# Kernel tuning notes

Hardware: AMD Instinct MI355X
Metric: run time of the kernel (lower is better)

The kernel has to match this reference:

```python
import jax, jax.numpy as jnp
import numpy as np

N_HEADS = 16
HEAD_DIM = 64
D_MODEL = N_HEADS * HEAD_DIM
MASK_NUM = -2.0**32 + 1.0
LN_EPS = 1e-8


def setup_inputs() -> dict:
    key = jax.random.key(0)
    ks = jax.random.split(key, 6)
    B, S = 2, 2048
    queries = jax.random.normal(ks[0], (B, S, D_MODEL), dtype=jnp.float32)
    keys = jax.random.normal(ks[1], (B, S, D_MODEL), dtype=jnp.float32)
    values = jax.random.normal(ks[2], (B, S, D_MODEL), dtype=jnp.float32)
    lim = np.sqrt(6.0 / (D_MODEL + D_MODEL)).astype(np.float32)  # glorot_uniform
    Wq = jax.random.uniform(ks[3], (D_MODEL, D_MODEL), jnp.float32, -lim, lim)
    Wk = jax.random.uniform(ks[4], (D_MODEL, D_MODEL), jnp.float32, -lim, lim)
    Wv = jax.random.uniform(ks[5], (D_MODEL, D_MODEL), jnp.float32, -lim, lim)
    gamma = jnp.ones((D_MODEL,), jnp.float32)
    beta = jnp.zeros((D_MODEL,), jnp.float32)
    return {"queries": queries, "keys": keys, "values": values,
            "Wq": Wq, "Wk": Wk, "Wv": Wv, "gamma": gamma, "beta": beta}


def _split_heads(x):
    # [B, S, H*dh] -> tf.split(axis=2)+concat(axis=0) order: [H*B, S, dh]
    B, S, _ = x.shape
    return x.reshape(B, S, N_HEADS, HEAD_DIM).transpose(2, 0, 1, 3).reshape(N_HEADS * B, S, HEAD_DIM)


def _merge_heads(x, B):
    # [H*B, S, dh] -> [B, S, H*dh]
    S = x.shape[1]
    return x.reshape(N_HEADS, B, S, HEAD_DIM).transpose(1, 2, 0, 3).reshape(B, S, D_MODEL)


def reference(queries, keys, values, Wq, Wk, Wv, gamma, beta):
    B = queries.shape[0]
    q = _split_heads(queries @ Wq)   # [HB, Sq, dh]
    k = _split_heads(keys @ Wk)      # [HB, Sk, dh]
    v = _split_heads(values @ Wv)    # [HB, Sk, dh]

    scores = jnp.einsum('bqd,bkd->bqk', q, k) / jnp.float32(np.sqrt(HEAD_DIM))
    # key padding mask: positions whose projected key is all-zero
    kmask = jnp.sign(jnp.sum(jnp.abs(k), axis=-1))  # [HB, Sk]
    scores = jnp.where(kmask[:, None, :] == 0, jnp.float32(MASK_NUM), scores)
    attn = jax.nn.softmax(scores, axis=-1)
    # query mask: zero out rows whose projected query is all-zero
    qmask = jnp.sign(jnp.sum(jnp.abs(q), axis=-1))  # [HB, Sq]
    attn = attn * qmask[:, :, None]
    att_out = jnp.einsum('bqk,bkd->bqd', attn, v)   # [HB, Sq, dh]
    att_out = _merge_heads(att_out, B)               # [B, Sq, D]

    x = att_out + queries
    mean = jnp.mean(x, axis=-1, keepdims=True)
    var = jnp.mean((x - mean) ** 2, axis=-1, keepdims=True)
    norm = (x - mean) / jnp.sqrt(var + LN_EPS)
    return gamma * norm + beta
```

## Files before the change

kernel.cpp:

```cpp
#include <hip/hip_runtime.h>

#define DM   1024
#define SEQ  2048
#define NH   16
#define HD   64
#define ROWS 4096

typedef unsigned short u16;
typedef unsigned int   u32;
typedef __attribute__((ext_vector_type(8))) __bf16 bf16x8;
typedef __attribute__((ext_vector_type(4))) float  f32x4;
typedef __attribute__((ext_vector_type(16))) float f32x16;

__device__ __forceinline__ u16 f2bf(float f) {
  u32 u = __builtin_bit_cast(u32, f);
  u += 0x7fffu + ((u >> 16) & 1u);
  return (u16)(u >> 16);
}

__device__ __forceinline__ void async16(const void* g, void* lds) {
  __builtin_amdgcn_global_load_lds((const __attribute__((address_space(1))) u32*)g,
                                   (__attribute__((address_space(3))) u32*)lds, 16, 0, 0);
}


__global__ __launch_bounds__(256) void k_cvt_act(const float* __restrict__ q,
                                                 const float* __restrict__ k,
                                                 const float* __restrict__ v,
                                                 u16* __restrict__ dst) {
  const float* src = blockIdx.z == 0 ? q : (blockIdx.z == 1 ? k : v);
  u16* d = dst + (size_t)blockIdx.z * ((size_t)ROWS * DM);
  size_t i = ((size_t)blockIdx.x * 256 + threadIdx.x) * 8;
  float4 a = *(const float4*)(src + i);
  float4 b = *(const float4*)(src + i + 4);
  u32 w0 = (u32)f2bf(a.x) | ((u32)f2bf(a.y) << 16);
  u32 w1 = (u32)f2bf(a.z) | ((u32)f2bf(a.w) << 16);
  u32 w2 = (u32)f2bf(b.x) | ((u32)f2bf(b.y) << 16);
  u32 w3 = (u32)f2bf(b.z) | ((u32)f2bf(b.w) << 16);
  uint4 o4; o4.x = w0; o4.y = w1; o4.z = w2; o4.w = w3;
  *(uint4*)(d + i) = o4;
}

__global__ __launch_bounds__(256) void k_cvt_wt(const float* __restrict__ Wq,
                                                const float* __restrict__ Wk,
                                                const float* __restrict__ Wv,
                                                u16* __restrict__ wt) {
  __shared__ float t[32][33];
  const float* W = blockIdx.z == 0 ? Wq : (blockIdx.z == 1 ? Wk : Wv);
  u16* D = wt + (size_t)blockIdx.z * (DM * DM);
  int bx = blockIdx.x * 32, by = blockIdx.y * 32;
  int x = threadIdx.x, y = threadIdx.y;
  for (int i = 0; i < 32; i += 8) t[y + i][x] = W[(size_t)(by + y + i) * DM + bx + x];
  __syncthreads();
  for (int i = 0; i < 32; i += 8) D[(size_t)(bx + y + i) * DM + by + x] = f2bf(t[x][y + i]);
}


__global__ __launch_bounds__(256) void k_gemm(const u16* __restrict__ Abase,
                                              const u16* __restrict__ Btbase,
                                              u16* __restrict__ Cbase) {
  __shared__ u16 As[128 * 32];
  __shared__ u16 Bs[128 * 32];
  const int z = blockIdx.z;
  const u16* A  = Abase  + (size_t)z * ((size_t)ROWS * DM);
  const u16* Bt = Btbase + (size_t)z * (DM * DM);
  u16* C        = Cbase  + (size_t)z * ((size_t)ROWS * DM);
  const float sc = (z == 0) ? 0.18033688011112043f : 1.0f;
  int tid = threadIdx.x, w = tid >> 6, l = tid & 63;
  int fr = l & 15, fq = l >> 4;
  int bid = blockIdx.y * 8 + blockIdx.x;
  int nb  = (bid & 7) * 32 + (bid >> 3);
  int m0 = (nb >> 3) * 128, n0 = (nb & 7) * 128;
  int wr = (w >> 1) * 64, wc = (w & 1) * 64;
  f32x4 acc[4][4];
  for (int i = 0; i < 4; ++i) for (int j = 0; j < 4; ++j) acc[i][j] = (f32x4){0.f, 0.f, 0.f, 0.f};

  for (int k0 = 0; k0 < DM; k0 += 32) {
    __syncthreads();
    for (int c = 0; c < 2; ++c) {
      int loff = (c * 4 + w) * 1024;
      int eoff = (loff >> 1) + l * 8;
      int row = eoff >> 5;
      int blk = (eoff & 31) >> 3;
      int gblk = blk ^ ((row >> 1) & 3);
      async16(A  + (size_t)(m0 + row) * DM + k0 + (gblk << 3), (char*)As + loff);
      async16(Bt + (size_t)(n0 + row) * DM + k0 + (gblk << 3), (char*)Bs + loff);
    }
    __syncthreads();
    bf16x8 af[4], bf[4];
    for (int i = 0; i < 4; ++i) {
      int row = wr + i * 16 + fr;
      af[i] = *(const bf16x8*)(As + row * 32 + ((fq ^ ((row >> 1) & 3)) << 3));
    }
    for (int j = 0; j < 4; ++j) {
      int row = wc + j * 16 + fr;
      bf[j] = *(const bf16x8*)(Bs + row * 32 + ((fq ^ ((row >> 1) & 3)) << 3));
    }
    for (int i = 0; i < 4; ++i)
      for (int j = 0; j < 4; ++j)
        acc[i][j] = __builtin_amdgcn_mfma_f32_16x16x32_bf16(af[i], bf[j], acc[i][j], 0, 0, 0);
  }
  for (int i = 0; i < 4; ++i)
    for (int j = 0; j < 4; ++j)
      for (int jj = 0; jj < 4; ++jj) {
        int row = m0 + wr + i * 16 + fq * 4 + jj;
        int col = n0 + wc + j * 16 + fr;
        C[(size_t)row * DM + col] = f2bf(acc[i][j][jj] * sc);
      }
}


__global__ __launch_bounds__(256) void k_vt(const u16* __restrict__ vproj,
                                            u16* __restrict__ vt) {
  __shared__ u16 t[64][64];
  int y = blockIdx.y;
  int h = y >> 1, b = y & 1;
  int s0 = blockIdx.x * 64;
  int tid = threadIdx.x;
  for (int c = 0; c < 2; ++c) {
    int rr = c * 32 + (tid >> 3);
    int blk = tid & 7;
    uint4 vv = *(const uint4*)(vproj + (size_t)(b * SEQ + s0 + rr) * DM + h * 64 + blk * 8);
    *(uint4*)(&t[rr][((blk ^ (rr & 7)) * 8)]) = vv;
  }
  __syncthreads();
  for (int c = 0; c < 2; ++c) {
    int d = c * 32 + (tid >> 3);
    int p = tid & 7;
    int B = p ^ (d & 7);
    int g = B >> 1, half = B & 1;
    u16 tmp[8];
    for (int j = 0; j < 8; ++j) {
      int kj = (j < 4) ? (4 * half + j) : (8 + 4 * half + (j - 4));
      int ss = 16 * g + kj;
      tmp[j] = t[ss][((d >> 3) ^ (ss & 7)) * 8 + (d & 7)];
    }
    *(uint4*)(vt + (size_t)(y * 64 + d) * SEQ + s0 + p * 8) = *(uint4*)tmp;
  }
}


__global__ __launch_bounds__(256, 2) void k_attn(const u16* __restrict__ Qp,
                                                 const u16* __restrict__ Kp,
                                                 const u16* __restrict__ Vt,
                                                 u16* __restrict__ attb) {
  __shared__ u16 lds[20480];
  const int tid = threadIdx.x, w = tid >> 6, l = tid & 63;
  const int lrow = l & 31, h = l >> 5;
  const int kh = w & 1, qg = w >> 1;
  const int g = blockIdx.x;
  const int vy = (g & 7) * 4 + ((g >> 3) & 3);
  const int vx = g >> 5;
  const int head = vy >> 1, b = vy & 1;
  const int hcol = head * 64;
  const int q0w = vx * 128 + qg * 64;

  bf16x8 qb00, qb01, qb02, qb03, qb10, qb11, qb12, qb13;
  {
    const u16* qr0 = Qp + (size_t)(b * SEQ + q0w + lrow) * DM + hcol + h * 8;
    qb00 = *(const bf16x8*)(qr0);
    qb01 = *(const bf16x8*)(qr0 + 16);
    qb02 = *(const bf16x8*)(qr0 + 32);
    qb03 = *(const bf16x8*)(qr0 + 48);
    const u16* qr1 = Qp + (size_t)(b * SEQ + q0w + 32 + lrow) * DM + hcol + h * 8;
    qb10 = *(const bf16x8*)(qr1);
    qb11 = *(const bf16x8*)(qr1 + 16);
    qb12 = *(const bf16x8*)(qr1 + 32);
    qb13 = *(const bf16x8*)(qr1 + 48);
  }

  const int sw = lrow & 7;
  const int kbase = kh * 4096 + lrow * 128;
  const int B0 = kbase + (((0 + h) ^ sw) << 4);
  const int B1 = kbase + (((2 + h) ^ sw) << 4);
  const int B2 = kbase + (((4 + h) ^ sw) << 4);
  const int B3 = kbase + (((6 + h) ^ sw) << 4);

  const int vfb = lrow * 128;
  const int V0 = vfb + (((4 * kh + 0 + h) ^ sw) << 4);
  const int V1 = vfb + (((4 * kh + 2 + h) ^ sw) << 4);

  const int ldo0 = w * 1024, ldo1 = (4 + w) * 1024;
  const int e0 = (ldo0 >> 1) + l * 8, e1 = (ldo1 >> 1) + l * 8;
  const int r0 = e0 >> 6, r1 = e1 >> 6;
  const int kb0 = ((e0 & 63) >> 3) ^ (r0 & 7), kb1 = ((e1 & 63) >> 3) ^ (r1 & 7);
  const u32 koff0 = (u32)((b * SEQ + r0) * DM + hcol + kb0 * 8);
  const u32 koff1 = (u32)((b * SEQ + r1) * DM + hcol + kb1 * 8);
  const u32 voff0 = (u32)((vy * 64 + r0) * SEQ + (e0 & 63));
  const u32 voff1 = (u32)((vy * 64 + r1) * SEQ + (e1 & 63));

  const f32x16 kzero = {};
  f32x16 ot00 = {}, ot01 = {}, ot10 = {}, ot11 = {};
  float lacc0 = 0.f, lacc1 = 0.f;
  bf16x8 pb00 = {}, pb01 = {}, pb10 = {}, pb11 = {};

  char* base = (char*)lds;
  async16(Kp + koff0, base + ldo0);
  async16(Kp + koff1, base + ldo1);
  async16(Vt + voff0, base + 16384 + ldo0);
  async16(Vt + voff1, base + 16384 + ldo1);

  int vwr = 1, vcr = 0, vrd = 2;
  for (int t = 0; t < SEQ / 64; ++t) {
    {
      u32 u = (t + 1 < SEQ / 64) ? (u32)(t + 1) : (u32)(SEQ / 64 - 1);
      u32 kadv = u * (64 * DM);
      u32 vadv = u * 64;
      char* kd = base + ((t + 1) & 1) * 8192;
      char* vd = base + 16384 + vwr * 8192;
      async16(Kp + kadv + koff0, kd + ldo0);
      async16(Kp + kadv + koff1, kd + ldo1);
      async16(Vt + vadv + voff0, vd + ldo0);
      async16(Vt + vadv + voff1, vd + ldo1);
    }
    asm volatile("s_waitcnt vmcnt(6)" ::: "memory");
    __builtin_amdgcn_s_barrier();
    asm volatile("" ::: "memory");

    const char* Kb = base + (t & 1) * 8192;
    bf16x8 a0 = *(const bf16x8*)(Kb + B0);
    bf16x8 a1 = *(const bf16x8*)(Kb + B1);
    bf16x8 a2 = *(const bf16x8*)(Kb + B2);
    bf16x8 a3 = *(const bf16x8*)(Kb + B3);
    __builtin_amdgcn_s_setprio(1);
    f32x16 st0 = __builtin_amdgcn_mfma_f32_32x32x16_bf16(a0, qb00, kzero, 0, 0, 0);
    f32x16 st1 = __builtin_amdgcn_mfma_f32_32x32x16_bf16(a0, qb10, kzero, 0, 0, 0);
    st0 = __builtin_amdgcn_mfma_f32_32x32x16_bf16(a1, qb01, st0, 0, 0, 0);
    st1 = __builtin_amdgcn_mfma_f32_32x32x16_bf16(a1, qb11, st1, 0, 0, 0);
    st0 = __builtin_amdgcn_mfma_f32_32x32x16_bf16(a2, qb02, st0, 0, 0, 0);
    st1 = __builtin_amdgcn_mfma_f32_32x32x16_bf16(a2, qb12, st1, 0, 0, 0);
    st0 = __builtin_amdgcn_mfma_f32_32x32x16_bf16(a3, qb03, st0, 0, 0, 0);
    st1 = __builtin_amdgcn_mfma_f32_32x32x16_bf16(a3, qb13, st1, 0, 0, 0);
    __builtin_amdgcn_s_setprio(0);

    if (t) {
      const char* Vb = base + 16384 + vrd * 8192;
      bf16x8 vf0 = *(const bf16x8*)(Vb + V0);
      bf16x8 vf1 = *(const bf16x8*)(Vb + V1);
      bf16x8 vf2 = *(const bf16x8*)(Vb + 4096 + V0);
      bf16x8 vf3 = *(const bf16x8*)(Vb + 4096 + V1);
      __builtin_amdgcn_s_setprio(1);
      ot00 = __builtin_amdgcn_mfma_f32_32x32x16_bf16(vf0, pb00, ot00, 0, 0, 0);
      ot10 = __builtin_amdgcn_mfma_f32_32x32x16_bf16(vf0, pb10, ot10, 0, 0, 0);
      ot00 = __builtin_amdgcn_mfma_f32_32x32x16_bf16(vf1, pb01, ot00, 0, 0, 0);
      ot10 = __builtin_amdgcn_mfma_f32_32x32x16_bf16(vf1, pb11, ot10, 0, 0, 0);
      ot01 = __builtin_amdgcn_mfma_f32_32x32x16_bf16(vf2, pb00, ot01, 0, 0, 0);
      ot11 = __builtin_amdgcn_mfma_f32_32x32x16_bf16(vf2, pb10, ot11, 0, 0, 0);
      ot01 = __builtin_amdgcn_mfma_f32_32x32x16_bf16(vf3, pb01, ot01, 0, 0, 0);
      ot11 = __builtin_amdgcn_mfma_f32_32x32x16_bf16(vf3, pb11, ot11, 0, 0, 0);
      __builtin_amdgcn_s_setprio(0);
    }

    {
      f32x16 p;
#pragma unroll
      for (int i = 0; i < 16; ++i) p[i] = __builtin_amdgcn_exp2f(st0[i]);
      float s0 = (p[0] + p[1]) + (p[2] + p[3]);
      float s1 = (p[4] + p[5]) + (p[6] + p[7]);
      float s2 = (p[8] + p[9]) + (p[10] + p[11]);
      float s3 = (p[12] + p[13]) + (p[14] + p[15]);
      lacc0 += (s0 + s1) + (s2 + s3);
#pragma unroll
      for (int j = 0; j < 8; ++j) { pb00[j] = (__bf16)p[j]; pb01[j] = (__bf16)p[8 + j]; }
    }
    {
      f32x16 p;
#pragma unroll
      for (int i = 0; i < 16; ++i) p[i] = __builtin_amdgcn_exp2f(st1[i]);
      float s0 = (p[0] + p[1]) + (p[2] + p[3]);
      float s1 = (p[4] + p[5]) + (p[6] + p[7]);
      float s2 = (p[8] + p[9]) + (p[10] + p[11]);
      float s3 = (p[12] + p[13]) + (p[14] + p[15]);
      lacc1 += (s0 + s1) + (s2 + s3);
#pragma unroll
      for (int j = 0; j < 8; ++j) { pb10[j] = (__bf16)p[j]; pb11[j] = (__bf16)p[8 + j]; }
    }

    asm volatile("" ::: "memory");
    __builtin_amdgcn_s_barrier();
    asm volatile("" ::: "memory");

    int tmp = vrd; vrd = vcr; vcr = vwr; vwr = tmp;
  }

  asm volatile("s_waitcnt vmcnt(0)" ::: "memory");
  __builtin_amdgcn_s_barrier();
  asm volatile("" ::: "memory");
  {
    const char* Vb = base + 16384 + vrd * 8192;
    bf16x8 vf0 = *(const bf16x8*)(Vb + V0);
    bf16x8 vf1 = *(const bf16x8*)(Vb + V1);
    bf16x8 vf2 = *(const bf16x8*)(Vb + 4096 + V0);
    bf16x8 vf3 = *(const bf16x8*)(Vb + 4096 + V1);
    ot00 = __builtin_amdgcn_mfma_f32_32x32x16_bf16(vf0, pb00, ot00, 0, 0, 0);
    ot10 = __builtin_amdgcn_mfma_f32_32x32x16_bf16(vf0, pb10, ot10, 0, 0, 0);
    ot00 = __builtin_amdgcn_mfma_f32_32x32x16_bf16(vf1, pb01, ot00, 0, 0, 0);
    ot10 = __builtin_amdgcn_mfma_f32_32x32x16_bf16(vf1, pb11, ot10, 0, 0, 0);
    ot01 = __builtin_amdgcn_mfma_f32_32x32x16_bf16(vf2, pb00, ot01, 0, 0, 0);
    ot11 = __builtin_amdgcn_mfma_f32_32x32x16_bf16(vf2, pb10, ot11, 0, 0, 0);
    ot01 = __builtin_amdgcn_mfma_f32_32x32x16_bf16(vf3, pb01, ot01, 0, 0, 0);
    ot11 = __builtin_amdgcn_mfma_f32_32x32x16_bf16(vf3, pb11, ot11, 0, 0, 0);
  }
  lacc0 += __shfl_xor(lacc0, 32);
  lacc1 += __shfl_xor(lacc1, 32);

  __syncthreads();
  float* mrg = (float*)lds;
  const int slot = qg * 4352;
  if (kh) {
#pragma unroll
    for (int r = 0; r < 16; ++r) {
      mrg[slot + r * 64 + l] = ot00[r];
      mrg[slot + (16 + r) * 64 + l] = ot01[r];
      mrg[slot + (32 + r) * 64 + l] = ot10[r];
      mrg[slot + (48 + r) * 64 + l] = ot11[r];
    }
    mrg[slot + 4096 + l] = lacc0;
    mrg[slot + 4160 + l] = lacc1;
  }
  __syncthreads();
  if (!kh) {
    float inv0 = 1.f / (lacc0 + mrg[slot + 4096 + l]);
    float inv1 = 1.f / (lacc1 + mrg[slot + 4160 + l]);
    u16* orow0 = attb + (size_t)(b * SEQ + q0w + lrow) * DM + hcol + 4 * h;
    u16* orow1 = attb + (size_t)(b * SEQ + q0w + 32 + lrow) * DM + hcol + 4 * h;
#pragma unroll
    for (int G = 0; G < 4; ++G) {
      uint2 o;
      o.x = (u32)f2bf((ot00[4*G+0] + mrg[slot + (4*G+0)*64 + l]) * inv0)
          | ((u32)f2bf((ot00[4*G+1] + mrg[slot + (4*G+1)*64 + l]) * inv0) << 16);
      o.y = (u32)f2bf((ot00[4*G+2] + mrg[slot + (4*G+2)*64 + l]) * inv0)
          | ((u32)f2bf((ot00[4*G+3] + mrg[slot + (4*G+3)*64 + l]) * inv0) << 16);
      *(uint2*)(orow0 + 8 * G) = o;
      uint2 o1;
      o1.x = (u32)f2bf((ot01[4*G+0] + mrg[slot + (16+4*G+0)*64 + l]) * inv0)
           | ((u32)f2bf((ot01[4*G+1] + mrg[slot + (16+4*G+1)*64 + l]) * inv0) << 16);
      o1.y = (u32)f2bf((ot01[4*G+2] + mrg[slot + (16+4*G+2)*64 + l]) * inv0)
           | ((u32)f2bf((ot01[4*G+3] + mrg[slot + (16+4*G+3)*64 + l]) * inv0) << 16);
      *(uint2*)(orow0 + 32 + 8 * G) = o1;
      uint2 o2;
      o2.x = (u32)f2bf((ot10[4*G+0] + mrg[slot + (32+4*G+0)*64 + l]) * inv1)
           | ((u32)f2bf((ot10[4*G+1] + mrg[slot + (32+4*G+1)*64 + l]) * inv1) << 16);
      o2.y = (u32)f2bf((ot10[4*G+2] + mrg[slot + (32+4*G+2)*64 + l]) * inv1)
           | ((u32)f2bf((ot10[4*G+3] + mrg[slot + (32+4*G+3)*64 + l]) * inv1) << 16);
      *(uint2*)(orow1 + 8 * G) = o2;
      uint2 o3;
      o3.x = (u32)f2bf((ot11[4*G+0] + mrg[slot + (48+4*G+0)*64 + l]) * inv1)
           | ((u32)f2bf((ot11[4*G+1] + mrg[slot + (48+4*G+1)*64 + l]) * inv1) << 16);
      o3.y = (u32)f2bf((ot11[4*G+2] + mrg[slot + (48+4*G+2)*64 + l]) * inv1)
           | ((u32)f2bf((ot11[4*G+3] + mrg[slot + (48+4*G+3)*64 + l]) * inv1) << 16);
      *(uint2*)(orow1 + 32 + 8 * G) = o3;
    }
  }
}


__global__ __launch_bounds__(256) void k_ln(const u16* __restrict__ attb,
                                            const float* __restrict__ qin,
                                            const float* __restrict__ gamma,
                                            const float* __restrict__ beta,
                                            float* __restrict__ out) {
  __shared__ float rsum[4], rsum2[4];
  int row = blockIdx.x, t = threadIdx.x;
  size_t off = (size_t)row * DM + t * 4;
  uint2 av = *(const uint2*)(attb + off);
  float4 a;
  a.x = __builtin_bit_cast(float, av.x << 16);
  a.y = __builtin_bit_cast(float, av.x & 0xffff0000u);
  a.z = __builtin_bit_cast(float, av.y << 16);
  a.w = __builtin_bit_cast(float, av.y & 0xffff0000u);
  float4 q = *(const float4*)(qin + off);
  float4 x; x.x = a.x + q.x; x.y = a.y + q.y; x.z = a.z + q.z; x.w = a.w + q.w;
  float s = x.x + x.y + x.z + x.w;
  float s2 = x.x * x.x + x.y * x.y + x.z * x.z + x.w * x.w;
  for (int o2 = 1; o2 < 64; o2 <<= 1) { s += __shfl_xor(s, o2); s2 += __shfl_xor(s2, o2); }
  int w = t >> 6, l = t & 63;
  if (l == 0) { rsum[w] = s; rsum2[w] = s2; }
  __syncthreads();
  s = rsum[0] + rsum[1] + rsum[2] + rsum[3];
  s2 = rsum2[0] + rsum2[1] + rsum2[2] + rsum2[3];
  float mean = s * (1.f / DM);
  float var = s2 * (1.f / DM) - mean * mean;
  float rstd = rsqrtf(var + 1e-8f);
  float4 g = *(const float4*)(gamma + t * 4);
  float4 be = *(const float4*)(beta + t * 4);
  float4 r;
  r.x = (x.x - mean) * rstd * g.x + be.x;
  r.y = (x.y - mean) * rstd * g.y + be.y;
  r.z = (x.z - mean) * rstd * g.z + be.z;
  r.w = (x.w - mean) * rstd * g.w + be.w;
  *(float4*)(out + off) = r;
}


extern "C" void kernel_launch(void* const* d_in, const int* in_sizes, int n_in,
                              void* d_out, int out_size, void* d_ws, size_t ws_size,
                              hipStream_t stream) {
  (void)in_sizes; (void)n_in; (void)out_size; (void)ws_size;
  const float* q     = (const float*)d_in[0];
  const float* k     = (const float*)d_in[1];
  const float* v     = (const float*)d_in[2];
  const float* Wq    = (const float*)d_in[3];
  const float* Wk    = (const float*)d_in[4];
  const float* Wv    = (const float*)d_in[5];
  const float* gamma = (const float*)d_in[6];
  const float* beta  = (const float*)d_in[7];
  float* out = (float*)d_out;
  char* ws = (char*)d_ws;

  const size_t ACT_B = 3ull * ROWS * DM * 2;
  const size_t WT_B  = 3ull * DM * DM * 2;

  u16* actb  = (u16*)ws;
  u16* wtb   = (u16*)(ws + ACT_B);
  u16* projb = (u16*)(ws + ACT_B + WT_B);
  u16* vt    = (u16*)ws;
  u16* attb  = (u16*)(ws + 8ull * 1024 * 1024);

  k_cvt_act<<<dim3(2048, 1, 3), 256, 0, stream>>>(q, k, v, actb);
  k_cvt_wt<<<dim3(32, 32, 3), dim3(32, 8), 0, stream>>>(Wq, Wk, Wv, wtb);
  k_gemm<<<dim3(8, 32, 3), 256, 0, stream>>>(actb, wtb, projb);
  k_vt<<<dim3(SEQ / 64, NH * 2), 256, 0, stream>>>(projb + 2ull * ROWS * DM, vt);
  k_attn<<<512, 256, 0, stream>>>(projb, projb + (size_t)ROWS * DM, vt, attb);
  k_ln<<<ROWS, 256, 0, stream>>>(attb, q, gamma, beta, out);
}
```

Measured before the change: 108.7 us.

## Enlarge projection GEMM tiles to 256x256 with double-buffered async LDS loads

The QKV projection GEMM now uses 512-thread blocks computing 256x256 output tiles with a K-step of 64, in place of 128x128 tiles with K-step 32. LDS is double-buffered so the next tile's global-to-LDS async loads are in flight during the MFMAs on the current tile, with partial vmcnt waits and raw barriers. s_setprio is raised around the MFMA bursts. The goal is better operand reuse and overlap of memory with compute. The cost is 128 KB of LDS per block and only 192 blocks over 256 CUs, so part of the GPU sits idle.

New measurement: 110.5 us. Within noise of the previous version (+1.7%).

```diff
diff --git a/kernel.cpp b/kernel.cpp
--- a/kernel.cpp
+++ b/kernel.cpp
@@ -56,51 +56,83 @@
 }
 
 
-__global__ __launch_bounds__(256) void k_gemm(const u16* __restrict__ Abase,
+__global__ __launch_bounds__(512) void k_gemm(const u16* __restrict__ Abase,
                                               const u16* __restrict__ Btbase,
                                               u16* __restrict__ Cbase) {
-  __shared__ u16 As[128 * 32];
-  __shared__ u16 Bs[128 * 32];
+  __shared__ u16 As[2][256 * 64];
+  __shared__ u16 Bs[2][256 * 64];
   const int z = blockIdx.z;
   const u16* A  = Abase  + (size_t)z * ((size_t)ROWS * DM);
   const u16* Bt = Btbase + (size_t)z * (DM * DM);
   u16* C        = Cbase  + (size_t)z * ((size_t)ROWS * DM);
   const float sc = (z == 0) ? 0.18033688011112043f : 1.0f;
-  int tid = threadIdx.x, w = tid >> 6, l = tid & 63;
-  int fr = l & 15, fq = l >> 4;
-  int bid = blockIdx.y * 8 + blockIdx.x;
-  int nb  = (bid & 7) * 32 + (bid >> 3);
-  int m0 = (nb >> 3) * 128, n0 = (nb & 7) * 128;
-  int wr = (w >> 1) * 64, wc = (w & 1) * 64;
-  f32x4 acc[4][4];
-  for (int i = 0; i < 4; ++i) for (int j = 0; j < 4; ++j) acc[i][j] = (f32x4){0.f, 0.f, 0.f, 0.f};
-
-  for (int k0 = 0; k0 < DM; k0 += 32) {
-    __syncthreads();
-    for (int c = 0; c < 2; ++c) {
-      int loff = (c * 4 + w) * 1024;
-      int eoff = (loff >> 1) + l * 8;
-      int row = eoff >> 5;
-      int blk = (eoff & 31) >> 3;
-      int gblk = blk ^ ((row >> 1) & 3);
-      async16(A  + (size_t)(m0 + row) * DM + k0 + (gblk << 3), (char*)As + loff);
-      async16(Bt + (size_t)(n0 + row) * DM + k0 + (gblk << 3), (char*)Bs + loff);
-    }
-    __syncthreads();
-    bf16x8 af[4], bf[4];
-    for (int i = 0; i < 4; ++i) {
-      int row = wr + i * 16 + fr;
-      af[i] = *(const bf16x8*)(As + row * 32 + ((fq ^ ((row >> 1) & 3)) << 3));
-    }
-    for (int j = 0; j < 4; ++j) {
-      int row = wc + j * 16 + fr;
-      bf[j] = *(const bf16x8*)(Bs + row * 32 + ((fq ^ ((row >> 1) & 3)) << 3));
-    }
-    for (int i = 0; i < 4; ++i)
-      for (int j = 0; j < 4; ++j)
-        acc[i][j] = __builtin_amdgcn_mfma_f32_16x16x32_bf16(af[i], bf[j], acc[i][j], 0, 0, 0);
-  }
-  for (int i = 0; i < 4; ++i)
+  const int tid = threadIdx.x, w = tid >> 6, l = tid & 63;
+  const int fr = l & 15, fq = l >> 4;
+  int bid = blockIdx.y * 4 + blockIdx.x;
+  int nb  = (bid & 7) * 8 + (bid >> 3);
+  int m0 = (nb >> 2) * 256, n0 = (nb & 3) * 256;
+  int wr = (w >> 2) * 128, wc = (w & 3) * 64;
+  f32x4 acc[8][4];
+  for (int i = 0; i < 8; ++i) for (int j = 0; j < 4; ++j) acc[i][j] = (f32x4){0.f, 0.f, 0.f, 0.f};
+
+  u32 aoff[4], boff[4];
+#pragma unroll
+  for (int i = 0; i < 4; ++i) {
+    int c = i * 512 + tid;
+    int row = c >> 3, blk = c & 7;
+    int gblk = blk ^ (row & 7);
+    aoff[i] = (u32)((m0 + row) * DM + gblk * 8);
+    boff[i] = (u32)((n0 + row) * DM + gblk * 8);
+  }
+
+#pragma unroll
+  for (int i = 0; i < 4; ++i) {
+    async16(A  + aoff[i], (char*)As[0] + (i * 512 + tid) * 16);
+    async16(Bt + boff[i], (char*)Bs[0] + (i * 512 + tid) * 16);
+  }
+
+  for (int t = 0; t < 16; ++t) {
+    const int cur = t & 1, nxt = cur ^ 1;
+    {
+      u32 kk = (t + 1 < 16) ? (u32)(t + 1) * 64u : 15u * 64u;
+#pragma unroll
+      for (int i = 0; i < 4; ++i) {
+        async16(A  + kk + aoff[i], (char*)As[nxt] + (i * 512 + tid) * 16);
+        async16(Bt + kk + boff[i], (char*)Bs[nxt] + (i * 512 + tid) * 16);
+      }
+    }
+    asm volatile("s_waitcnt vmcnt(8)" ::: "memory");
+    __builtin_amdgcn_s_barrier();
+    asm volatile("" ::: "memory");
+
+#pragma unroll
+    for (int ks = 0; ks < 2; ++ks) {
+      bf16x8 af[8], bf[4];
+#pragma unroll
+      for (int i = 0; i < 8; ++i) {
+        int row = wr + i * 16 + fr;
+        af[i] = *(const bf16x8*)(&As[cur][row * 64 + (((ks * 4 + fq) ^ (row & 7)) << 3)]);
+      }
+#pragma unroll
+      for (int j = 0; j < 4; ++j) {
+        int row = wc + j * 16 + fr;
+        bf[j] = *(const bf16x8*)(&Bs[cur][row * 64 + (((ks * 4 + fq) ^ (row & 7)) << 3)]);
+      }
+      __builtin_amdgcn_s_setprio(1);
+#pragma unroll
+      for (int i = 0; i < 8; ++i)
+#pragma unroll
+        for (int j = 0; j < 4; ++j)
+          acc[i][j] = __builtin_amdgcn_mfma_f32_16x16x32_bf16(af[i], bf[j], acc[i][j], 0, 0, 0);
+      __builtin_amdgcn_s_setprio(0);
+    }
+
+    asm volatile("" ::: "memory");
+    __builtin_amdgcn_s_barrier();
+    asm volatile("" ::: "memory");
+  }
+
+  for (int i = 0; i < 8; ++i)
     for (int j = 0; j < 4; ++j)
       for (int jj = 0; jj < 4; ++jj) {
         int row = m0 + wr + i * 16 + fq * 4 + jj;
@@ -419,7 +451,7 @@
 
   k_cvt_act<<<dim3(2048, 1, 3), 256, 0, stream>>>(q, k, v, actb);
   k_cvt_wt<<<dim3(32, 32, 3), dim3(32, 8), 0, stream>>>(Wq, Wk, Wv, wtb);
-  k_gemm<<<dim3(8, 32, 3), 256, 0, stream>>>(actb, wtb, projb);
+  k_gemm<<<dim3(4, 16, 3), 512, 0, stream>>>(actb, wtb, projb);
   k_vt<<<dim3(SEQ / 64, NH * 2), 256, 0, stream>>>(projb + 2ull * ROWS * DM, vt);
   k_attn<<<512, 256, 0, stream>>>(projb, projb + (size_t)ROWS * DM, vt, attb);
   k_ln<<<ROWS, 256, 0, stream>>>(attb, q, gamma, beta, out);
```
